# Kernel optimization log

Hardware: AMD Instinct MI355X
Metric: run time of the kernel (lower is better)

## Reference

```python
import jax, jax.numpy as jnp
import numpy as np

EPS = 1e-8

def rmsnorm(x, w):
    norm = jax.lax.rsqrt(jnp.mean(x * x, axis=-1, keepdims=True) + EPS)
    return x * norm * w

def setup_inputs() -> dict:
    key = jax.random.key(0)
    ks = jax.random.split(key, 10)
    B, L, D, S = 8, 4096, 1024, 256
    sD = 1.0 / np.sqrt(D)
    sS = 1.0 / np.sqrt(S)
    return {
        "x": jax.random.normal(ks[0], (B, L, D), jnp.float32),
        "w_norm": jnp.ones((D,), jnp.float32),
        "W_in": jax.random.normal(ks[1], (D, 3 * S), jnp.float32) * sD,
        "b_in": jnp.zeros((3 * S,), jnp.float32),
        "W_x": jax.random.normal(ks[2], (S, S), jnp.float32) * sS,
        "b_x": jnp.zeros((S,), jnp.float32),
        "W_dt": jax.random.normal(ks[3], (S, S), jnp.float32) * sS,
        "b_dt": jnp.zeros((S,), jnp.float32),
        "W_out": jax.random.normal(ks[4], (S, D), jnp.float32) * sS,
        "b_out": jnp.zeros((D,), jnp.float32),
    }

def reference(x, w_norm, W_in, b_in, W_x, b_x, W_dt, b_dt, W_out, b_out):
    # MambaLikeBlock forward (dropout=0 / eval mode)
    residual = x
    xn = rmsnorm(x, w_norm)
    uzg = xn @ W_in + b_in                       # [B,L,3S]
    S = uzg.shape[-1] // 3
    u, z, g = uzg[..., :S], uzg[..., S:2 * S], uzg[..., 2 * S:]
    # per-step projections are time-independent -> precompute for all t
    ut = jnp.tanh(u @ W_x + b_x)                 # [B,L,S]
    dt = jax.nn.sigmoid(z @ W_dt + b_dt)         # [B,L,S]

    def step(h, inp):
        u_t, dt_t = inp
        h = (1.0 - dt_t) * h + dt_t * u_t
        return h, h

    h0 = jnp.zeros(ut.shape[::2][::-1][:0] + (ut.shape[0], ut.shape[2]), ut.dtype)  # [B,S]
    _, hs = jax.lax.scan(step, h0, (ut.transpose(1, 0, 2), dt.transpose(1, 0, 2)))
    hs = hs.transpose(1, 0, 2)                   # [B,L,S]
    y = hs * jax.nn.sigmoid(g)
    y = y @ W_out + b_out                        # [B,L,D]
    return residual + y
```

## Files before the change

kernel.cpp:

```cpp
#include <hip/hip_runtime.h>
#include <hip/hip_bf16.h>

#define BB 8
#define LL 4096
#define DD 1024
#define SS 256
#define NTOK (BB * LL)
#define CCH 64
#define TCH (LL / CCH)

typedef short bf16x8 __attribute__((ext_vector_type(8)));
typedef float f32x4 __attribute__((ext_vector_type(4)));

__device__ __forceinline__ float bfu(unsigned short v) {
  union { unsigned int i; float f; } x;
  x.i = ((unsigned int)v) << 16;
  return x.f;
}

__global__ __launch_bounds__(256) void prep_rms(const float* __restrict__ x,
                                                const float* __restrict__ wn,
                                                __hip_bfloat16* __restrict__ xn) {
  const size_t row = blockIdx.x;
  const int t = threadIdx.x;
  const float4 xv = reinterpret_cast<const float4*>(x + row * DD)[t];
  const float4 wv = reinterpret_cast<const float4*>(wn)[t];
  float ss = xv.x * xv.x + xv.y * xv.y + xv.z * xv.z + xv.w * xv.w;
#pragma unroll
  for (int m = 32; m >= 1; m >>= 1) ss += __shfl_xor(ss, m);
  __shared__ float red[4];
  if ((t & 63) == 0) red[t >> 6] = ss;
  __syncthreads();
  const float tot = red[0] + red[1] + red[2] + red[3];
  const float r = rsqrtf(tot * (1.0f / DD) + 1e-8f);
  union { ushort4 u; __hip_bfloat16 h[4]; } o;
  o.h[0] = __float2bfloat16(xv.x * wv.x * r);
  o.h[1] = __float2bfloat16(xv.y * wv.y * r);
  o.h[2] = __float2bfloat16(xv.z * wv.z * r);
  o.h[3] = __float2bfloat16(xv.w * wv.w * r);
  reinterpret_cast<ushort4*>(xn + row * DD)[t] = o.u;
}

__global__ __launch_bounds__(256) void convT(const float* __restrict__ W,
                                             __hip_bfloat16* __restrict__ WT,
                                             int K, int Nw) {
  const int idx = blockIdx.x * 256 + threadIdx.x;
  if (idx >= K * Nw) return;
  const int k = idx / Nw, n = idx % Nw;
  WT[(size_t)n * K + k] = __float2bfloat16(W[idx]);
}

template <int EPI>
__global__ __launch_bounds__(256) void gemm_bf16(
    const __hip_bfloat16* __restrict__ A, int lda,
    const __hip_bfloat16* __restrict__ BT,
    const float* __restrict__ bias,
    void* __restrict__ Cptr, int ldc,
    const float* __restrict__ resid,
    int M, int Nt, int K) {
  __shared__ __align__(16) __hip_bfloat16 As[128][72];
  __shared__ __align__(16) __hip_bfloat16 Bs[128][72];

  const int t = threadIdx.x;
  const int bm = blockIdx.x, bn = blockIdx.y;
  const int wave = t >> 6, lane = t & 63;
  const int wr = (wave >> 1) * 64;
  const int wc = (wave & 1) * 64;
  const int lr = lane & 15;
  const int kg = lane >> 4;

  const int tr = t >> 3;
  const int tc = (t & 7) * 8;

  f32x4 acc[4][4] = {};

  for (int k0 = 0; k0 < K; k0 += 64) {
    __syncthreads();
#pragma unroll
    for (int p = 0; p < 4; ++p) {
      const int r = p * 32 + tr;
      const int4 va = *reinterpret_cast<const int4*>(
          A + (size_t)(bm * 128 + r) * lda + k0 + tc);
      *reinterpret_cast<int4*>(&As[r][tc]) = va;
      const int4 vb = *reinterpret_cast<const int4*>(
          BT + (size_t)(bn * 128 + r) * K + k0 + tc);
      *reinterpret_cast<int4*>(&Bs[r][tc]) = vb;
    }
    __syncthreads();
#pragma unroll
    for (int kk = 0; kk < 64; kk += 32) {
      bf16x8 af[4], bfr[4];
#pragma unroll
      for (int m = 0; m < 4; ++m)
        af[m] = *reinterpret_cast<const bf16x8*>(&As[wr + m * 16 + lr][kk + kg * 8]);
#pragma unroll
      for (int n = 0; n < 4; ++n)
        bfr[n] = *reinterpret_cast<const bf16x8*>(&Bs[wc + n * 16 + lr][kk + kg * 8]);
#pragma unroll
      for (int m = 0; m < 4; ++m)
#pragma unroll
        for (int n = 0; n < 4; ++n)
          acc[m][n] = __builtin_amdgcn_mfma_f32_16x16x32_bf16(af[m], bfr[n],
                                                              acc[m][n], 0, 0, 0);
    }
  }

  const int rowb = bm * 128 + wr + kg * 4;
  const int colb = bn * 128 + wc + lr;
#pragma unroll
  for (int m = 0; m < 4; ++m) {
#pragma unroll
    for (int n = 0; n < 4; ++n) {
      const int col = colb + n * 16;
      const float bv = bias[col];
#pragma unroll
      for (int j = 0; j < 4; ++j) {
        const int row = rowb + m * 16 + j;
        float v = acc[m][n][j] + bv;
        if (EPI == 0) {
          ((__hip_bfloat16*)Cptr)[(size_t)row * ldc + col] = __float2bfloat16(v);
        } else if (EPI == 1) {
          ((__hip_bfloat16*)Cptr)[(size_t)row * ldc + col] = __float2bfloat16(tanhf(v));
        } else if (EPI == 2) {
          ((__hip_bfloat16*)Cptr)[(size_t)row * ldc + col] =
              __float2bfloat16(1.0f / (1.0f + expf(-v)));
        } else {
          const size_t off = (size_t)row * ldc + col;
          ((float*)Cptr)[off] = v + resid[off];
        }
      }
    }
  }
}

__global__ __launch_bounds__(128) void scan_phase_a(
    const __hip_bfloat16* __restrict__ ut,
    const __hip_bfloat16* __restrict__ dtb,
    float* __restrict__ h0s, float* __restrict__ As) {
  const int bc = blockIdx.x;
  const int b = bc / CCH, c = bc % CCH;
  const int ch = threadIdx.x * 2;
  const size_t base = ((size_t)b * LL + (size_t)c * TCH) * SS + ch;
  float h0 = 0.f, h1 = 0.f, A0 = 1.f, A1 = 1.f;
#pragma unroll 8
  for (int t = 0; t < TCH; ++t) {
    const ushort2 uu = *reinterpret_cast<const ushort2*>(ut + base + (size_t)t * SS);
    const ushort2 dd = *reinterpret_cast<const ushort2*>(dtb + base + (size_t)t * SS);
    const float d0 = bfu(dd.x), d1 = bfu(dd.y);
    h0 = fmaf(d0, bfu(uu.x) - h0, h0);
    h1 = fmaf(d1, bfu(uu.y) - h1, h1);
    A0 *= (1.f - d0);
    A1 *= (1.f - d1);
  }
  const size_t o = (size_t)bc * SS + ch;
  *reinterpret_cast<float2*>(h0s + o) = make_float2(h0, h1);
  *reinterpret_cast<float2*>(As + o) = make_float2(A0, A1);
}

__global__ __launch_bounds__(256) void scan_phase_b(
    const float* __restrict__ h0s, const float* __restrict__ As,
    float* __restrict__ hins) {
  const int b = blockIdx.x;
  const int s = threadIdx.x;
  float hin = 0.f;
#pragma unroll 8
  for (int c = 0; c < CCH; ++c) {
    const size_t idx = ((size_t)b * CCH + c) * SS + s;
    hins[idx] = hin;
    hin = fmaf(As[idx], hin, h0s[idx]);
  }
}

__global__ __launch_bounds__(128) void scan_phase_c(
    const __hip_bfloat16* __restrict__ ut,
    const __hip_bfloat16* __restrict__ dtb,
    const __hip_bfloat16* __restrict__ gz,
    const float* __restrict__ hins,
    __hip_bfloat16* __restrict__ hsg) {
  const int bc = blockIdx.x;
  const int b = bc / CCH, c = bc % CCH;
  const int ch = threadIdx.x * 2;
  const size_t rowbase = (size_t)b * LL + (size_t)c * TCH;
  const float2 hv = *reinterpret_cast<const float2*>(hins + (size_t)bc * SS + ch);
  float h0 = hv.x, h1 = hv.y;
#pragma unroll 8
  for (int t = 0; t < TCH; ++t) {
    const size_t row = rowbase + t;
    const ushort2 uu = *reinterpret_cast<const ushort2*>(ut + row * SS + ch);
    const ushort2 dd = *reinterpret_cast<const ushort2*>(dtb + row * SS + ch);
    const ushort2 gg = *reinterpret_cast<const ushort2*>(gz + row * 768 + ch);
    h0 = fmaf(bfu(dd.x), bfu(uu.x) - h0, h0);
    h1 = fmaf(bfu(dd.y), bfu(uu.y) - h1, h1);
    union { ushort2 u; __hip_bfloat16 h[2]; } o;
    o.h[0] = __float2bfloat16(h0 / (1.f + expf(-bfu(gg.x))));
    o.h[1] = __float2bfloat16(h1 / (1.f + expf(-bfu(gg.y))));
    *reinterpret_cast<ushort2*>(hsg + row * SS + ch) = o.u;
  }
}

extern "C" void kernel_launch(void* const* d_in, const int* in_sizes, int n_in,
                              void* d_out, int out_size, void* d_ws, size_t ws_size,
                              hipStream_t stream) {
  const float* x      = (const float*)d_in[0];
  const float* w_norm = (const float*)d_in[1];
  const float* W_in   = (const float*)d_in[2];
  const float* b_in   = (const float*)d_in[3];
  const float* W_x    = (const float*)d_in[4];
  const float* b_x    = (const float*)d_in[5];
  const float* W_dt   = (const float*)d_in[6];
  const float* b_dt   = (const float*)d_in[7];
  const float* W_out  = (const float*)d_in[8];
  const float* b_out  = (const float*)d_in[9];
  float* out = (float*)d_out;

  char* w = (char*)d_ws;
  __hip_bfloat16* xn  = (__hip_bfloat16*)w;
  __hip_bfloat16* ut  = (__hip_bfloat16*)w;
  __hip_bfloat16* dtb = (__hip_bfloat16*)(w + (size_t)NTOK * SS * 2);
  w += (size_t)NTOK * DD * 2;
  __hip_bfloat16* uzg = (__hip_bfloat16*)w;  w += (size_t)NTOK * 768 * 2;
  __hip_bfloat16* WinT  = (__hip_bfloat16*)w;  w += (size_t)768 * DD * 2;
  __hip_bfloat16* WxT   = (__hip_bfloat16*)w;  w += (size_t)SS * SS * 2;
  __hip_bfloat16* WdtT  = (__hip_bfloat16*)w;  w += (size_t)SS * SS * 2;
  __hip_bfloat16* WoutT = (__hip_bfloat16*)w;  w += (size_t)DD * SS * 2;
  float* h0s  = (float*)w;  w += (size_t)BB * CCH * SS * 4;
  float* As   = (float*)w;  w += (size_t)BB * CCH * SS * 4;
  float* hins = (float*)w;  w += (size_t)BB * CCH * SS * 4;
  (void)ws_size; (void)n_in; (void)in_sizes; (void)out_size;

  convT<<<(DD * 768 + 255) / 256, 256, 0, stream>>>(W_in, WinT, DD, 768);
  convT<<<(SS * SS + 255) / 256, 256, 0, stream>>>(W_x, WxT, SS, SS);
  convT<<<(SS * SS + 255) / 256, 256, 0, stream>>>(W_dt, WdtT, SS, SS);
  convT<<<(SS * DD + 255) / 256, 256, 0, stream>>>(W_out, WoutT, SS, DD);

  prep_rms<<<NTOK, 256, 0, stream>>>(x, w_norm, xn);

  gemm_bf16<0><<<dim3(NTOK / 128, 768 / 128), 256, 0, stream>>>(
      xn, DD, WinT, b_in, uzg, 768, nullptr, NTOK, 768, DD);

  gemm_bf16<1><<<dim3(NTOK / 128, SS / 128), 256, 0, stream>>>(
      uzg, 768, WxT, b_x, ut, SS, nullptr, NTOK, SS, SS);
  gemm_bf16<2><<<dim3(NTOK / 128, SS / 128), 256, 0, stream>>>(
      uzg + SS, 768, WdtT, b_dt, dtb, SS, nullptr, NTOK, SS, SS);

  scan_phase_a<<<BB * CCH, 128, 0, stream>>>(ut, dtb, h0s, As);
  scan_phase_b<<<BB, 256, 0, stream>>>(h0s, As, hins);
  scan_phase_c<<<BB * CCH, 128, 0, stream>>>(ut, dtb, uzg + 2 * SS, hins, ut);

  gemm_bf16<3><<<dim3(NTOK / 128, DD / 128), 256, 0, stream>>>(
      ut, SS, WoutT, b_out, out, DD, x, NTOK, DD, SS);
}
```

Measured before the change: 288.2 us.

## Use direct global-to-LDS loads in GEMM and vectorize transposed-MFMA epilogue

The GEMM tile loads now use global_load_lds to write straight from global memory into unpadded shared memory instead of going through registers. The MFMA operands are swapped so each lane holds four consecutive output columns, which lets the epilogue use float4 bias and residual loads and vector stores. The four weight-transpose launches are merged into one kernel. Dropping the padding may bring back LDS bank conflicts on the fragment reads.

```diff
diff --git a/kernel.cpp b/kernel.cpp
--- a/kernel.cpp
+++ b/kernel.cpp
@@ -16,6 +16,12 @@
   union { unsigned int i; float f; } x;
   x.i = ((unsigned int)v) << 16;
   return x.f;
+}
+
+__device__ __forceinline__ void gl_lds16(const __hip_bfloat16* g, void* l) {
+  __builtin_amdgcn_global_load_lds(
+      (const __attribute__((address_space(1))) unsigned int*)g,
+      (__attribute__((address_space(3))) unsigned int*)l, 16, 0, 0);
 }
 
 __global__ __launch_bounds__(256) void prep_rms(const float* __restrict__ x,
@@ -41,13 +47,20 @@
   reinterpret_cast<ushort4*>(xn + row * DD)[t] = o.u;
 }
 
-__global__ __launch_bounds__(256) void convT(const float* __restrict__ W,
-                                             __hip_bfloat16* __restrict__ WT,
-                                             int K, int Nw) {
+__global__ __launch_bounds__(256) void convT4(
+    const float* __restrict__ W0, const float* __restrict__ W1,
+    const float* __restrict__ W2, const float* __restrict__ W3,
+    __hip_bfloat16* __restrict__ T0, __hip_bfloat16* __restrict__ T1,
+    __hip_bfloat16* __restrict__ T2, __hip_bfloat16* __restrict__ T3) {
+  const int seg = blockIdx.y;
+  const int K = (seg == 0) ? DD : SS;
+  const int Nw = (seg == 0) ? 768 : (seg == 3) ? DD : SS;
+  const float* W = (seg == 0) ? W0 : (seg == 1) ? W1 : (seg == 2) ? W2 : W3;
+  __hip_bfloat16* T = (seg == 0) ? T0 : (seg == 1) ? T1 : (seg == 2) ? T2 : T3;
   const int idx = blockIdx.x * 256 + threadIdx.x;
   if (idx >= K * Nw) return;
   const int k = idx / Nw, n = idx % Nw;
-  WT[(size_t)n * K + k] = __float2bfloat16(W[idx]);
+  T[(size_t)n * K + k] = __float2bfloat16(W[idx]);
 }
 
 template <int EPI>
@@ -57,9 +70,9 @@
     const float* __restrict__ bias,
     void* __restrict__ Cptr, int ldc,
     const float* __restrict__ resid,
-    int M, int Nt, int K) {
-  __shared__ __align__(16) __hip_bfloat16 As[128][72];
-  __shared__ __align__(16) __hip_bfloat16 Bs[128][72];
+    int K) {
+  __shared__ __align__(16) __hip_bfloat16 As[128][64];
+  __shared__ __align__(16) __hip_bfloat16 Bs[128][64];
 
   const int t = threadIdx.x;
   const int bm = blockIdx.x, bn = blockIdx.y;
@@ -69,8 +82,12 @@
   const int lr = lane & 15;
   const int kg = lane >> 4;
 
-  const int tr = t >> 3;
-  const int tc = (t & 7) * 8;
+  const int g_row = wave * 32 + (lane >> 3);
+  const int g_col = (lane & 7) * 8;
+  const __hip_bfloat16* Ab = A + (size_t)(bm * 128 + g_row) * lda + g_col;
+  const __hip_bfloat16* Bb = BT + (size_t)(bn * 128 + g_row) * K + g_col;
+  char* lAs = (char*)(&As[0][0]) + (size_t)(wave * 32) * 128;
+  char* lBs = (char*)(&Bs[0][0]) + (size_t)(wave * 32) * 128;
 
   f32x4 acc[4][4] = {};
 
@@ -78,13 +95,8 @@
     __syncthreads();
 #pragma unroll
     for (int p = 0; p < 4; ++p) {
-      const int r = p * 32 + tr;
-      const int4 va = *reinterpret_cast<const int4*>(
-          A + (size_t)(bm * 128 + r) * lda + k0 + tc);
-      *reinterpret_cast<int4*>(&As[r][tc]) = va;
-      const int4 vb = *reinterpret_cast<const int4*>(
-          BT + (size_t)(bn * 128 + r) * K + k0 + tc);
-      *reinterpret_cast<int4*>(&Bs[r][tc]) = vb;
+      gl_lds16(Ab + (size_t)(p * 8) * lda + k0, lAs + p * 1024);
+      gl_lds16(Bb + (size_t)(p * 8) * K + k0, lBs + p * 1024);
     }
     __syncthreads();
 #pragma unroll
@@ -100,34 +112,42 @@
       for (int m = 0; m < 4; ++m)
 #pragma unroll
         for (int n = 0; n < 4; ++n)
-          acc[m][n] = __builtin_amdgcn_mfma_f32_16x16x32_bf16(af[m], bfr[n],
+          acc[m][n] = __builtin_amdgcn_mfma_f32_16x16x32_bf16(bfr[n], af[m],
                                                               acc[m][n], 0, 0, 0);
     }
   }
 
-  const int rowb = bm * 128 + wr + kg * 4;
-  const int colb = bn * 128 + wc + lr;
+  const int row0 = bm * 128 + wr + lr;
+  const int col0 = bn * 128 + wc + kg * 4;
 #pragma unroll
   for (int m = 0; m < 4; ++m) {
+    const int row = row0 + m * 16;
 #pragma unroll
     for (int n = 0; n < 4; ++n) {
-      const int col = colb + n * 16;
-      const float bv = bias[col];
-#pragma unroll
-      for (int j = 0; j < 4; ++j) {
-        const int row = rowb + m * 16 + j;
-        float v = acc[m][n][j] + bv;
-        if (EPI == 0) {
-          ((__hip_bfloat16*)Cptr)[(size_t)row * ldc + col] = __float2bfloat16(v);
-        } else if (EPI == 1) {
-          ((__hip_bfloat16*)Cptr)[(size_t)row * ldc + col] = __float2bfloat16(tanhf(v));
+      const int colb = col0 + n * 16;
+      const float4 bv = *reinterpret_cast<const float4*>(&bias[colb]);
+      float v0 = acc[m][n][0] + bv.x;
+      float v1 = acc[m][n][1] + bv.y;
+      float v2 = acc[m][n][2] + bv.z;
+      float v3 = acc[m][n][3] + bv.w;
+      if (EPI == 3) {
+        const size_t off = (size_t)row * ldc + colb;
+        const float4 rv = *reinterpret_cast<const float4*>(&resid[off]);
+        float4 ov;
+        ov.x = v0 + rv.x; ov.y = v1 + rv.y; ov.z = v2 + rv.z; ov.w = v3 + rv.w;
+        *reinterpret_cast<float4*>(&((float*)Cptr)[off]) = ov;
+      } else {
+        if (EPI == 1) {
+          v0 = tanhf(v0); v1 = tanhf(v1); v2 = tanhf(v2); v3 = tanhf(v3);
         } else if (EPI == 2) {
-          ((__hip_bfloat16*)Cptr)[(size_t)row * ldc + col] =
-              __float2bfloat16(1.0f / (1.0f + expf(-v)));
-        } else {
-          const size_t off = (size_t)row * ldc + col;
-          ((float*)Cptr)[off] = v + resid[off];
+          v0 = 1.f / (1.f + expf(-v0)); v1 = 1.f / (1.f + expf(-v1));
+          v2 = 1.f / (1.f + expf(-v2)); v3 = 1.f / (1.f + expf(-v3));
         }
+        union { ushort4 u; __hip_bfloat16 h[4]; } o;
+        o.h[0] = __float2bfloat16(v0); o.h[1] = __float2bfloat16(v1);
+        o.h[2] = __float2bfloat16(v2); o.h[3] = __float2bfloat16(v3);
+        *reinterpret_cast<ushort4*>(
+            &((__hip_bfloat16*)Cptr)[(size_t)row * ldc + colb]) = o.u;
       }
     }
   }
@@ -228,25 +248,23 @@
   float* hins = (float*)w;  w += (size_t)BB * CCH * SS * 4;
   (void)ws_size; (void)n_in; (void)in_sizes; (void)out_size;
 
-  convT<<<(DD * 768 + 255) / 256, 256, 0, stream>>>(W_in, WinT, DD, 768);
-  convT<<<(SS * SS + 255) / 256, 256, 0, stream>>>(W_x, WxT, SS, SS);
-  convT<<<(SS * SS + 255) / 256, 256, 0, stream>>>(W_dt, WdtT, SS, SS);
-  convT<<<(SS * DD + 255) / 256, 256, 0, stream>>>(W_out, WoutT, SS, DD);
+  convT4<<<dim3((DD * 768 + 255) / 256, 4), 256, 0, stream>>>(
+      W_in, W_x, W_dt, W_out, WinT, WxT, WdtT, WoutT);
 
   prep_rms<<<NTOK, 256, 0, stream>>>(x, w_norm, xn);
 
   gemm_bf16<0><<<dim3(NTOK / 128, 768 / 128), 256, 0, stream>>>(
-      xn, DD, WinT, b_in, uzg, 768, nullptr, NTOK, 768, DD);
+      xn, DD, WinT, b_in, uzg, 768, nullptr, DD);
 
   gemm_bf16<1><<<dim3(NTOK / 128, SS / 128), 256, 0, stream>>>(
-      uzg, 768, WxT, b_x, ut, SS, nullptr, NTOK, SS, SS);
+      uzg, 768, WxT, b_x, ut, SS, nullptr, SS);
   gemm_bf16<2><<<dim3(NTOK / 128, SS / 128), 256, 0, stream>>>(
-      uzg + SS, 768, WdtT, b_dt, dtb, SS, nullptr, NTOK, SS, SS);
+      uzg + SS, 768, WdtT, b_dt, dtb, SS, nullptr, SS);
 
   scan_phase_a<<<BB * CCH, 128, 0, stream>>>(ut, dtb, h0s, As);
   scan_phase_b<<<BB, 256, 0, stream>>>(h0s, As, hins);
   scan_phase_c<<<BB * CCH, 128, 0, stream>>>(ut, dtb, uzg + 2 * SS, hins, ut);
 
   gemm_bf16<3><<<dim3(NTOK / 128, DD / 128), 256, 0, stream>>>(
-      ut, SS, WoutT, b_out, out, DD, x, NTOK, DD, SS);
-}
+      ut, SS, WoutT, b_out, out, DD, x, SS);
+}
```

Measured after the change: 297.8 us. +3.3%, slower.
